# Kernel optimization log

Measured on AMD Instinct MI355X. Metric: run time of the kernel, lower is better.

The kernel has to match this reference:

```python
import jax, jax.numpy as jnp
import numpy as np

N = 100000   # nodes
E = 1600000  # edges
D = 128      # input feature dim
H = 128      # hidden dim
C = 40       # output classes


def _gcn_conv(x, W, b, src, dst, norm):
    # PyG GCNConv: h = x @ W; out_i = sum_j (d_i^-1/2 d_j^-1/2) h_j over in-edges,
    # including self-loops, then + bias. norm = deg^-1/2 with self-loop-augmented degree.
    h = x @ W                                    # [N, H]
    coef = norm[src] * norm[dst]                 # [E]
    agg = jax.ops.segment_sum(h[src] * coef[:, None], dst, num_segments=N)
    agg = agg + h * (norm * norm)[:, None]       # self-loop term
    return agg + b


def setup_inputs() -> dict:
    key = jax.random.key(0)
    ks = jax.random.split(key, 12)
    x = jax.random.normal(ks[0], (N, D), dtype=jnp.float32)
    edge_index = jax.random.randint(ks[1], (2, E), 0, N, dtype=jnp.int64)

    def lin(k, fan_in, fan_out):
        s = 1.0 / np.sqrt(fan_in)
        return jax.random.uniform(k, (fan_in, fan_out), jnp.float32, -s, s)

    return {
        "x": x,
        "edge_index": edge_index,
        "W1": lin(ks[2], D, H), "b1": jnp.zeros((H,), jnp.float32),
        "W2": lin(ks[3], H, H), "b2": jnp.zeros((H,), jnp.float32),
        "W3": lin(ks[4], H, H), "b3": jnp.zeros((H,), jnp.float32),
        "Wp1": lin(ks[5], H, H), "bp1": jnp.zeros((H,), jnp.float32),
        "Wp2": lin(ks[6], H, C), "bp2": jnp.zeros((C,), jnp.float32),
    }


def reference(x, edge_index, W1, b1, W2, b2, W3, b3, Wp1, bp1, Wp2, bp2):
    src, dst = edge_index[0], edge_index[1]
    # degree with self-loops (GCNConv adds self-loops by default)
    deg = jax.ops.segment_sum(jnp.ones((E,), jnp.float32), dst, num_segments=N) + 1.0
    norm = jax.lax.rsqrt(deg)                    # deg^-1/2

    h = x
    for W, b in ((W1, b1), (W2, b2), (W3, b3)):
        h = _gcn_conv(h, W, b, src, dst, norm)
        h = jax.nn.relu(h)
        # dropout is a no-op at inference / rate 0

    h = h @ Wp1 + bp1
    h = h @ Wp2 + bp2
    return jax.nn.log_softmax(h, axis=1)
```

## Files before the change

### kernel.cpp

```cpp
#include <hip/hip_runtime.h>
#include <hip/hip_bf16.h>
#include <math.h>


#define DH 128
#define NC 40
#define BN 128
#define MAXNB 1024
#define CAP 2560
#define CH 4096
#define SP 136

typedef __attribute__((ext_vector_type(8))) short bf16x8;
typedef __attribute__((ext_vector_type(4))) float f32x4;

__device__ __forceinline__ unsigned short f2bf(float f) {
    unsigned u = __float_as_uint(f);
    unsigned r = (u + 0x7fffu + ((u >> 16) & 1u)) >> 16;
    return (unsigned short)r;
}
__device__ __forceinline__ unsigned pack2(float lo, float hi) {
    return (unsigned)f2bf(lo) | ((unsigned)f2bf(hi) << 16);
}


__global__ __launch_bounds__(256) void init_bpos(unsigned* __restrict__ bpos, int NB) {
    int i = blockIdx.x * 256 + threadIdx.x;
    if (i < NB) bpos[i] = (unsigned)i * CAP;
}


__global__ __launch_bounds__(256) void bucket_scatter(const int* __restrict__ src,
                                                      const int* __restrict__ dst, int E,
                                                      unsigned* __restrict__ bpos,
                                                      unsigned* __restrict__ ebuf) {
    __shared__ unsigned hist[MAXNB];
    __shared__ unsigned gbase[MAXNB];
    __shared__ unsigned lim[MAXNB];
    __shared__ unsigned cur[MAXNB];
    int tid = threadIdx.x;
    int e0 = blockIdx.x * CH;
    int nE = min(CH, E - e0);
    int nE4 = nE & ~3;

    for (int i = tid; i < MAXNB; i += 256) { hist[i] = 0; cur[i] = 0; }
    __syncthreads();
    for (int i = tid * 4; i < nE4; i += 1024) {
        int4 dv = *(const int4*)(dst + e0 + i);
        atomicAdd(&hist[(unsigned)dv.x >> 7], 1u);
        atomicAdd(&hist[(unsigned)dv.y >> 7], 1u);
        atomicAdd(&hist[(unsigned)dv.z >> 7], 1u);
        atomicAdd(&hist[(unsigned)dv.w >> 7], 1u);
    }
    for (int i = nE4 + tid; i < nE; i += 256)
        atomicAdd(&hist[(unsigned)dst[e0 + i] >> 7], 1u);
    __syncthreads();
    for (int i = tid; i < MAXNB; i += 256) {
        unsigned h = hist[i];
        if (h) {
            unsigned o = atomicAdd(&bpos[i], h);
            gbase[i] = o;
            lim[i] = min(o + h, (unsigned)(i + 1) * CAP);
        }
    }
    __syncthreads();
    for (int i = tid * 4; i < nE4; i += 1024) {
        int4 sv = *(const int4*)(src + e0 + i);
        int4 dv = *(const int4*)(dst + e0 + i);
        {
            unsigned b = (unsigned)dv.x >> 7;
            unsigned p = gbase[b] + atomicAdd(&cur[b], 1u);
            if (p < lim[b]) ebuf[p] = ((unsigned)sv.x << 7) | ((unsigned)dv.x & 127u);
        }
        {
            unsigned b = (unsigned)dv.y >> 7;
            unsigned p = gbase[b] + atomicAdd(&cur[b], 1u);
            if (p < lim[b]) ebuf[p] = ((unsigned)sv.y << 7) | ((unsigned)dv.y & 127u);
        }
        {
            unsigned b = (unsigned)dv.z >> 7;
            unsigned p = gbase[b] + atomicAdd(&cur[b], 1u);
            if (p < lim[b]) ebuf[p] = ((unsigned)sv.z << 7) | ((unsigned)dv.z & 127u);
        }
        {
            unsigned b = (unsigned)dv.w >> 7;
            unsigned p = gbase[b] + atomicAdd(&cur[b], 1u);
            if (p < lim[b]) ebuf[p] = ((unsigned)sv.w << 7) | ((unsigned)dv.w & 127u);
        }
    }
    for (int i = nE4 + tid; i < nE; i += 256) {
        int s = src[e0 + i];
        int d = dst[e0 + i];
        unsigned b = (unsigned)d >> 7;
        unsigned p = gbase[b] + atomicAdd(&cur[b], 1u);
        if (p < lim[b]) ebuf[p] = ((unsigned)s << 7) | ((unsigned)d & 127u);
    }
}


__global__ __launch_bounds__(256) void bucket_degfill(const unsigned* __restrict__ ebuf,
                                                      const unsigned* __restrict__ bpos,
                                                      unsigned* __restrict__ cnt,
                                                      float* __restrict__ nrm,
                                                      unsigned* __restrict__ offN,
                                                      unsigned* __restrict__ dh,
                                                      int* __restrict__ csr, int N) {
    __shared__ unsigned h[BN], lb[BN], cur[BN];
    __shared__ int lcsr[CAP];
    __shared__ unsigned dhh[256];
    __shared__ unsigned tot;

    int b = blockIdx.x, tid = threadIdx.x;
    unsigned ebase = (unsigned)b * CAP;
    unsigned used = min(bpos[b] - ebase, (unsigned)CAP);
    unsigned used4 = used & ~3u;

    if (tid < BN) { h[tid] = 0; cur[tid] = 0; }
    dhh[tid] = 0;
    if (tid == 0) tot = 0;
    __syncthreads();

    for (unsigned i = tid * 4; i < used4; i += 1024) {
        uint4 v = *(const uint4*)(ebuf + ebase + i);
        atomicAdd(&h[v.x & 127u], 1u);
        atomicAdd(&h[v.y & 127u], 1u);
        atomicAdd(&h[v.z & 127u], 1u);
        atomicAdd(&h[v.w & 127u], 1u);
    }
    for (unsigned i = used4 + tid; i < used; i += 256)
        atomicAdd(&h[ebuf[ebase + i] & 127u], 1u);
    __syncthreads();

    if (tid < BN) {
        unsigned m = h[tid];
        lb[tid] = m ? atomicAdd(&tot, m) : 0u;
    }
    __syncthreads();

    for (unsigned i = tid * 4; i < used4; i += 1024) {
        uint4 v = *(const uint4*)(ebuf + ebase + i);
        {
            unsigned nl = v.x & 127u;
            unsigned r = atomicAdd(&cur[nl], 1u);
            lcsr[lb[nl] + r] = (int)(v.x >> 7);
        }
        {
            unsigned nl = v.y & 127u;
            unsigned r = atomicAdd(&cur[nl], 1u);
            lcsr[lb[nl] + r] = (int)(v.y >> 7);
        }
        {
            unsigned nl = v.z & 127u;
            unsigned r = atomicAdd(&cur[nl], 1u);
            lcsr[lb[nl] + r] = (int)(v.z >> 7);
        }
        {
            unsigned nl = v.w & 127u;
            unsigned r = atomicAdd(&cur[nl], 1u);
            lcsr[lb[nl] + r] = (int)(v.w >> 7);
        }
    }
    for (unsigned i = used4 + tid; i < used; i += 256) {
        unsigned v = ebuf[ebase + i];
        unsigned nl = v & 127u;
        unsigned r = atomicAdd(&cur[nl], 1u);
        lcsr[lb[nl] + r] = (int)(v >> 7);
    }

    if (tid < BN) {
        int node = b * BN + tid;
        if (node < N) {
            unsigned m = h[tid];
            cnt[node] = m;
            nrm[node] = rsqrtf((float)m + 1.0f);
            offN[node] = ebase + lb[tid];
            atomicAdd(&dhh[min(m, 255u)], 1u);
        }
    }
    __syncthreads();

    for (unsigned i = tid * 4; i < used4; i += 1024)
        *(int4*)(csr + ebase + i) = *(const int4*)&lcsr[i];
    for (unsigned i = used4 + tid; i < used; i += 256)
        csr[ebase + i] = lcsr[i];
    if (dhh[tid]) atomicAdd(&dh[tid], dhh[tid]);
}


__global__ __launch_bounds__(256) void deg_scatter(const unsigned* __restrict__ cnt, int N,
                                                   const unsigned* __restrict__ dh,
                                                   unsigned* __restrict__ binpos,
                                                   const unsigned* __restrict__ offN,
                                                   int* __restrict__ perm,
                                                   unsigned* __restrict__ pd2) {
    __shared__ unsigned hh[256], base[256], cur[256], sdh[256], sns[256];
    int t = threadIdx.x;
    hh[t] = 0; cur[t] = 0; sdh[t] = dh[t];
    __syncthreads();
    unsigned ns = 0;
    for (int d = t + 1; d < 256; ++d) ns += sdh[d];
    sns[t] = ns;
    int i = blockIdx.x * 256 + t;
    unsigned d = 0;
    if (i < N) { d = min(cnt[i], 255u); atomicAdd(&hh[d], 1u); }
    __syncthreads();
    if (hh[t]) base[t] = sns[t] + atomicAdd(&binpos[t], hh[t]);
    __syncthreads();
    if (i < N) {
        unsigned r = atomicAdd(&cur[d], 1u);
        unsigned idx = base[d] + r;
        perm[idx] = i;
        pd2[idx] = (offN[i] << 9) | min(cnt[i], 511u);
    }
}


__global__ __launch_bounds__(256) void prep_w(const float* __restrict__ W1,
                                              const float* __restrict__ W2,
                                              const float* __restrict__ W3,
                                              const float* __restrict__ Wp1,
                                              const float* __restrict__ bp1,
                                              const float* __restrict__ Wp2,
                                              const float* __restrict__ bp2,
                                              unsigned short* __restrict__ Wt,
                                              unsigned short* __restrict__ Wft,
                                              float* __restrict__ bfh) {
    int id = blockIdx.x * 256 + threadIdx.x;
    if (id < 3 * DH * DH) {
        int l = id >> 14, r = id & (DH * DH - 1);
        int k = r >> 7, n = r & 127;
        const float* W = (l == 0) ? W1 : (l == 1) ? W2 : W3;
        Wt[l * DH * DH + n * DH + k] = f2bf(W[k * DH + n]);
    } else if (id < 3 * DH * DH + 48 * DH) {
        int o = id - 3 * DH * DH;
        int c = o >> 7, k = o & 127;
        float acc = 0.f;
        if (c < NC)
            for (int j = 0; j < DH; ++j) acc += Wp1[k * DH + j] * Wp2[j * NC + c];
        Wft[c * DH + k] = f2bf(acc);
    } else if (id < 3 * DH * DH + 48 * DH + 48) {
        int c = id - 3 * DH * DH - 48 * DH;
        float acc = 0.f;
        if (c < NC) {
            acc = bp2[c];
            for (int j = 0; j < DH; ++j) acc += bp1[j] * Wp2[j * NC + c];
        }
        bfh[c] = acc;
    }
}


__global__ __launch_bounds__(256) void gemm_mfma_f32(const float* __restrict__ X,
                                                     const unsigned short* __restrict__ Wt,
                                                     const float* __restrict__ nrm,
                                                     unsigned short* __restrict__ outb,
                                                     int nrows) {
    const int tid = threadIdx.x;
    const int wave = tid >> 6;
    const int lane = tid & 63;
    const int m = lane & 15;
    const int quad = lane >> 4;
    const int rbase = blockIdx.x * 128 + wave * 32;

    union U8 { bf16x8 v; unsigned u[4]; };

    f32x4 acc[2][8];
#pragma unroll
    for (int rt = 0; rt < 2; ++rt)
#pragma unroll
        for (int ct = 0; ct < 8; ++ct) acc[rt][ct] = (f32x4){0.f, 0.f, 0.f, 0.f};

#pragma unroll
    for (int kt = 0; kt < 4; ++kt) {
        const int kof = kt * 32 + quad * 8;
        bf16x8 a[2], b[8];
#pragma unroll
        for (int rt = 0; rt < 2; ++rt) {
            int r = rbase + rt * 16 + m;
            r = (r < nrows) ? r : (nrows - 1);
            const float* p = X + (size_t)r * DH + kof;
            float4 u0 = *(const float4*)p;
            float4 u1 = *(const float4*)(p + 4);
            U8 t;
            t.u[0] = pack2(u0.x, u0.y);
            t.u[1] = pack2(u0.z, u0.w);
            t.u[2] = pack2(u1.x, u1.y);
            t.u[3] = pack2(u1.z, u1.w);
            a[rt] = t.v;
        }
#pragma unroll
        for (int ct = 0; ct < 8; ++ct)
            b[ct] = *(const bf16x8*)(Wt + (ct * 16 + m) * DH + kof);
#pragma unroll
        for (int rt = 0; rt < 2; ++rt)
#pragma unroll
            for (int ct = 0; ct < 8; ++ct)
                acc[rt][ct] = __builtin_amdgcn_mfma_f32_16x16x32_bf16(a[rt], b[ct], acc[rt][ct], 0, 0, 0);
    }

#pragma unroll
    for (int rt = 0; rt < 2; ++rt)
#pragma unroll
        for (int reg = 0; reg < 4; ++reg) {
            int r = rbase + rt * 16 + quad * 4 + reg;
            if (r < nrows) {
                float s = nrm[r];
#pragma unroll
                for (int ct = 0; ct < 8; ++ct)
                    outb[(size_t)r * DH + ct * 16 + m] = f2bf(acc[rt][ct][reg] * s);
            }
        }
}


__device__ __forceinline__ void bf8_add(float* acc, uint4 v) {
    acc[0] += __uint_as_float(v.x << 16);
    acc[1] += __uint_as_float(v.x & 0xffff0000u);
    acc[2] += __uint_as_float(v.y << 16);
    acc[3] += __uint_as_float(v.y & 0xffff0000u);
    acc[4] += __uint_as_float(v.z << 16);
    acc[5] += __uint_as_float(v.z & 0xffff0000u);
    acc[6] += __uint_as_float(v.w << 16);
    acc[7] += __uint_as_float(v.w & 0xffff0000u);
}

__device__ __forceinline__ void gather_phase(const uint4* __restrict__ Abf,
                                             const int* __restrict__ csr,
                                             const unsigned* __restrict__ pd2,
                                             const int* __restrict__ perm,
                                             const float* __restrict__ bias,
                                             unsigned short (*sA)[SP],
                                             int* snode, float* snrm, int N) {
    const int tid = threadIdx.x;
    const int g = tid >> 4;
    const int lane = tid & 15;
    const int idx = blockIdx.x * 16 + g;
    if (idx < N) {
        const unsigned pd = pd2[idx];
        const unsigned o = pd >> 9;
        const unsigned d = pd & 511u;
        const int node = perm[idx];

        int i0 = 0, i1 = 0, i2 = 0, i3 = 0;
        if ((unsigned)lane < d)      i0 = csr[o + lane];
        if ((unsigned)(16 + lane) < d) i1 = csr[o + 16 + lane];
        if ((unsigned)(32 + lane) < d) i2 = csr[o + 32 + lane];
        if ((unsigned)(48 + lane) < d) i3 = csr[o + 48 + lane];

        float acc[8];
        {
            uint4 v = Abf[(size_t)node * 16 + lane];
            acc[0] = __uint_as_float(v.x << 16);
            acc[1] = __uint_as_float(v.x & 0xffff0000u);
            acc[2] = __uint_as_float(v.y << 16);
            acc[3] = __uint_as_float(v.y & 0xffff0000u);
            acc[4] = __uint_as_float(v.z << 16);
            acc[5] = __uint_as_float(v.z & 0xffff0000u);
            acc[6] = __uint_as_float(v.w << 16);
            acc[7] = __uint_as_float(v.w & 0xffff0000u);
        }

        const unsigned dl = min(d, 64u);
        const int sb = g << 4;
        unsigned e = 0;
        for (; e + 4 <= dl; e += 4) {
            int rsel = (e < 16) ? i0 : (e < 32) ? i1 : (e < 48) ? i2 : i3;
            int bb = sb + (int)(e & 15u);
            int s0 = __shfl(rsel, bb + 0);
            int s1 = __shfl(rsel, bb + 1);
            int s2 = __shfl(rsel, bb + 2);
            int s3 = __shfl(rsel, bb + 3);
            uint4 v0 = Abf[(size_t)s0 * 16 + lane];
            uint4 v1 = Abf[(size_t)s1 * 16 + lane];
            uint4 v2 = Abf[(size_t)s2 * 16 + lane];
            uint4 v3 = Abf[(size_t)s3 * 16 + lane];
            bf8_add(acc, v0);
            bf8_add(acc, v1);
            bf8_add(acc, v2);
            bf8_add(acc, v3);
        }
        for (; e < dl; ++e) {
            int rsel = (e < 16) ? i0 : (e < 32) ? i1 : (e < 48) ? i2 : i3;
            int s = __shfl(rsel, sb + (int)(e & 15u));
            uint4 v = Abf[(size_t)s * 16 + lane];
            bf8_add(acc, v);
        }
        for (; e < d; ++e) {
            int s = csr[o + e];
            uint4 v = Abf[(size_t)s * 16 + lane];
            bf8_add(acc, v);
        }

        float nm = rsqrtf((float)d + 1.0f);
        if (lane == 0) { snode[g] = node; snrm[g] = nm; }
        float4 b0 = *(const float4*)(bias + lane * 8);
        float4 b1 = *(const float4*)(bias + lane * 8 + 4);
        uint4 ov;
        ov.x = pack2(fmaxf(acc[0] * nm + b0.x, 0.f), fmaxf(acc[1] * nm + b0.y, 0.f));
        ov.y = pack2(fmaxf(acc[2] * nm + b0.z, 0.f), fmaxf(acc[3] * nm + b0.w, 0.f));
        ov.z = pack2(fmaxf(acc[4] * nm + b1.x, 0.f), fmaxf(acc[5] * nm + b1.y, 0.f));
        ov.w = pack2(fmaxf(acc[6] * nm + b1.z, 0.f), fmaxf(acc[7] * nm + b1.w, 0.f));
        *(uint4*)&sA[g][lane * 8] = ov;
    }
    __syncthreads();
}


__global__ __launch_bounds__(256, 8) void agg_gemm(const uint4* __restrict__ Abf,
                                                   const int* __restrict__ csr,
                                                   const unsigned* __restrict__ pd2,
                                                   const int* __restrict__ perm,
                                                   const float* __restrict__ bias,
                                                   const unsigned short* __restrict__ Wt,
                                                   unsigned short* __restrict__ outb, int N) {
    __shared__ unsigned short sA[16][SP];
    __shared__ int snode[16];
    __shared__ float snrm[16];
    gather_phase(Abf, csr, pd2, perm, bias, sA, snode, snrm, N);

    const int tid = threadIdx.x;
    const int wave = tid >> 6;
    const int l64 = tid & 63;
    const int m = l64 & 15;
    const int quad = l64 >> 4;

    f32x4 acc[2];
    acc[0] = (f32x4){0.f, 0.f, 0.f, 0.f};
    acc[1] = (f32x4){0.f, 0.f, 0.f, 0.f};

#pragma unroll
    for (int kt = 0; kt < 4; ++kt) {
        const int kof = kt * 32 + quad * 8;
        bf16x8 a = *(const bf16x8*)&sA[m][kof];
#pragma unroll
        for (int c2 = 0; c2 < 2; ++c2) {
            const int ct = wave * 2 + c2;
            bf16x8 b = *(const bf16x8*)(Wt + (ct * 16 + m) * DH + kof);
            acc[c2] = __builtin_amdgcn_mfma_f32_16x16x32_bf16(a, b, acc[c2], 0, 0, 0);
        }
    }

#pragma unroll
    for (int reg = 0; reg < 4; ++reg) {
        int idx = blockIdx.x * 16 + quad * 4 + reg;
        if (idx < N) {
            int r = snode[quad * 4 + reg];
            float s = snrm[quad * 4 + reg];
#pragma unroll
            for (int c2 = 0; c2 < 2; ++c2)
                outb[(size_t)r * DH + (wave * 2 + c2) * 16 + m] = f2bf(acc[c2][reg] * s);
        }
    }
}


__global__ __launch_bounds__(256, 8) void agg_head(const uint4* __restrict__ Abf,
                                                   const int* __restrict__ csr,
                                                   const unsigned* __restrict__ pd2,
                                                   const int* __restrict__ perm,
                                                   const float* __restrict__ bias,
                                                   const unsigned short* __restrict__ Wft,
                                                   const float* __restrict__ bfh,
                                                   float* __restrict__ out, int N) {
    __shared__ unsigned short sA[16][SP];
    __shared__ int snode[16];
    __shared__ float snrm[16];
    gather_phase(Abf, csr, pd2, perm, bias, sA, snode, snrm, N);

    const int tid = threadIdx.x;
    if (tid >= 64) return;
    const int m = tid & 15;
    const int quad = tid >> 4;

    f32x4 acc[3];
#pragma unroll
    for (int ct = 0; ct < 3; ++ct) acc[ct] = (f32x4){0.f, 0.f, 0.f, 0.f};

#pragma unroll
    for (int kt = 0; kt < 4; ++kt) {
        const int kof = kt * 32 + quad * 8;
        bf16x8 a = *(const bf16x8*)&sA[m][kof];
#pragma unroll
        for (int ct = 0; ct < 3; ++ct) {
            bf16x8 b = *(const bf16x8*)(Wft + (ct * 16 + m) * DH + kof);
            acc[ct] = __builtin_amdgcn_mfma_f32_16x16x32_bf16(a, b, acc[ct], 0, 0, 0);
        }
    }

    float bias0 = bfh[m];
    float bias1 = bfh[16 + m];
    float bias2 = bfh[32 + m];

#pragma unroll
    for (int reg = 0; reg < 4; ++reg) {
        float v0 = acc[0][reg] + bias0;
        float v1 = acc[1][reg] + bias1;
        float v2 = (m < 8) ? (acc[2][reg] + bias2) : -1e30f;
        float mx = fmaxf(fmaxf(v0, v1), v2);
#pragma unroll
        for (int dlt = 1; dlt < 16; dlt <<= 1) mx = fmaxf(mx, __shfl_xor(mx, dlt));
        float s = __expf(v0 - mx) + __expf(v1 - mx) + ((m < 8) ? __expf(v2 - mx) : 0.f);
#pragma unroll
        for (int dlt = 1; dlt < 16; dlt <<= 1) s += __shfl_xor(s, dlt);
        float ls = mx + __logf(s);
        int idx = blockIdx.x * 16 + quad * 4 + reg;
        if (idx < N) {
            int r = snode[quad * 4 + reg];
            out[(size_t)r * NC + m] = v0 - ls;
            out[(size_t)r * NC + 16 + m] = v1 - ls;
            if (m < 8) out[(size_t)r * NC + 32 + m] = v2 - ls;
        }
    }
}


extern "C" void kernel_launch(void* const* d_in, const int* in_sizes, int n_in,
                              void* d_out, int out_size, void* d_ws, size_t ws_size,
                              hipStream_t stream) {
    const float* x   = (const float*)d_in[0];
    const int*   ei  = (const int*)d_in[1];
    const float* W1  = (const float*)d_in[2];
    const float* b1  = (const float*)d_in[3];
    const float* W2  = (const float*)d_in[4];
    const float* b2  = (const float*)d_in[5];
    const float* W3  = (const float*)d_in[6];
    const float* b3  = (const float*)d_in[7];
    const float* Wp1 = (const float*)d_in[8];
    const float* bp1 = (const float*)d_in[9];
    const float* Wp2 = (const float*)d_in[10];
    const float* bp2 = (const float*)d_in[11];
    float* out = (float*)d_out;

    const int N = in_sizes[0] / DH;
    const int E = in_sizes[1] / 2;
    const int* src = ei;
    const int* dst = ei + E;
    const int NB = (N + BN - 1) / BN;

    char* w = (char*)d_ws;
    unsigned short* Ab  = (unsigned short*)w; w += (size_t)N * DH * 2;
    unsigned short* Bb  = (unsigned short*)w; w += (size_t)N * DH * 2;
    int*      csr    = (int*)w;      w += (size_t)NB * CAP * 4;
    unsigned* ebuf   = (unsigned*)w; w += (size_t)NB * CAP * 4;
    unsigned* dh     = (unsigned*)w; w += 256 * 4;
    unsigned* binpos = (unsigned*)w; w += 256 * 4;
    unsigned* bpos   = (unsigned*)w; w += MAXNB * 4;
    unsigned* cnt    = (unsigned*)w; w += (size_t)N * 4;
    float*    nrm    = (float*)w;    w += (size_t)N * 4;
    unsigned* offN   = (unsigned*)w; w += (size_t)N * 4;
    unsigned* pd2    = (unsigned*)w; w += (size_t)((N + 31) & ~31) * 4;
    int*      perm   = (int*)w;      w += (size_t)((N + 31) & ~31) * 4;
    unsigned short* Wt  = (unsigned short*)w; w += 3 * DH * DH * 2;
    unsigned short* Wft = (unsigned short*)w; w += 48 * DH * 2;
    float*    bfh    = (float*)w;    w += 64 * 4;

    const int gC = (E + CH - 1) / CH;
    const int gN = (N + 255) / 256;

    hipMemsetAsync(dh, 0, 256 * 4 + 256 * 4, stream);
    init_bpos     <<<(NB + 255) / 256, 256, 0, stream>>>(bpos, NB);
    bucket_scatter<<<gC, 256, 0, stream>>>(src, dst, E, bpos, ebuf);
    bucket_degfill<<<NB, 256, 0, stream>>>(ebuf, bpos, cnt, nrm, offN, dh, csr, N);
    deg_scatter   <<<gN, 256, 0, stream>>>(cnt, N, dh, binpos, offN, perm, pd2);
    prep_w<<<(3 * DH * DH + 48 * DH + 48 + 255) / 256, 256, 0, stream>>>(
        W1, W2, W3, Wp1, bp1, Wp2, bp2, Wt, Wft, bfh);

    const int gG = (N + 127) / 128;
    const int gF = (N + 15) / 16;

    gemm_mfma_f32<<<gG, 256, 0, stream>>>(x, Wt, nrm, Ab, N);
    agg_gemm<<<gF, 256, 0, stream>>>((const uint4*)Ab, csr, pd2, perm, b1,
                                     Wt + DH * DH, Bb, N);
    agg_gemm<<<gF, 256, 0, stream>>>((const uint4*)Bb, csr, pd2, perm, b2,
                                     Wt + 2 * DH * DH, Ab, N);
    agg_head<<<gF, 256, 0, stream>>>((const uint4*)Ab, csr, pd2, perm, b3,
                                     Wft, bfh, out, N);
}
```

Before: 380.1 us.

## Merge weight prep into bucket scatter, drop init kernel, shrink GEMM tile

Folds the weight-prep kernel into the bucket scatter launch as extra blocks and replaces the bpos init kernel with a memset, so bucket offsets are now stored relative to each bucket's base. This removes two launches and their serialization gaps. The first-layer GEMM now gives each wave one 16-row tile instead of two, which doubles the grid and lowers register pressure. The explicit occupancy hint of 8 is also removed from the aggregation kernels, which may change their register allocation.

```diff
diff --git a/kernel.cpp b/kernel.cpp
--- a/kernel.cpp
+++ b/kernel.cpp
@@ -24,24 +24,49 @@
 }
 
 
-__global__ __launch_bounds__(256) void init_bpos(unsigned* __restrict__ bpos, int NB) {
-    int i = blockIdx.x * 256 + threadIdx.x;
-    if (i < NB) bpos[i] = (unsigned)i * CAP;
-}
-
-
-__global__ __launch_bounds__(256) void bucket_scatter(const int* __restrict__ src,
-                                                      const int* __restrict__ dst, int E,
-                                                      unsigned* __restrict__ bpos,
-                                                      unsigned* __restrict__ ebuf) {
+__global__ __launch_bounds__(256) void bucket_scatter_prep(
+        const int* __restrict__ src, const int* __restrict__ dst, int E,
+        unsigned* __restrict__ bpos, unsigned* __restrict__ ebuf,
+        const float* __restrict__ W1, const float* __restrict__ W2,
+        const float* __restrict__ W3, const float* __restrict__ Wp1,
+        const float* __restrict__ bp1, const float* __restrict__ Wp2,
+        const float* __restrict__ bp2, unsigned short* __restrict__ Wt,
+        unsigned short* __restrict__ Wft, float* __restrict__ bfh, int gC) {
     __shared__ unsigned hist[MAXNB];
     __shared__ unsigned gbase[MAXNB];
     __shared__ unsigned lim[MAXNB];
     __shared__ unsigned cur[MAXNB];
-    int tid = threadIdx.x;
-    int e0 = blockIdx.x * CH;
-    int nE = min(CH, E - e0);
-    int nE4 = nE & ~3;
+    const int tid = threadIdx.x;
+
+    if (blockIdx.x >= gC) {
+        int id = (blockIdx.x - gC) * 256 + tid;
+        if (id < 3 * DH * DH) {
+            int l = id >> 14, r = id & (DH * DH - 1);
+            int k = r >> 7, n = r & 127;
+            const float* W = (l == 0) ? W1 : (l == 1) ? W2 : W3;
+            Wt[l * DH * DH + n * DH + k] = f2bf(W[k * DH + n]);
+        } else if (id < 3 * DH * DH + 48 * DH) {
+            int o = id - 3 * DH * DH;
+            int c = o >> 7, k = o & 127;
+            float acc = 0.f;
+            if (c < NC)
+                for (int j = 0; j < DH; ++j) acc += Wp1[k * DH + j] * Wp2[j * NC + c];
+            Wft[c * DH + k] = f2bf(acc);
+        } else if (id < 3 * DH * DH + 48 * DH + 48) {
+            int c = id - 3 * DH * DH - 48 * DH;
+            float acc = 0.f;
+            if (c < NC) {
+                acc = bp2[c];
+                for (int j = 0; j < DH; ++j) acc += bp1[j] * Wp2[j * NC + c];
+            }
+            bfh[c] = acc;
+        }
+        return;
+    }
+
+    const int e0 = blockIdx.x * CH;
+    const int nE = min(CH, E - e0);
+    const int nE4 = nE & ~3;
 
     for (int i = tid; i < MAXNB; i += 256) { hist[i] = 0; cur[i] = 0; }
     __syncthreads();
@@ -58,7 +83,7 @@
     for (int i = tid; i < MAXNB; i += 256) {
         unsigned h = hist[i];
         if (h) {
-            unsigned o = atomicAdd(&bpos[i], h);
+            unsigned o = (unsigned)i * CAP + atomicAdd(&bpos[i], h);
             gbase[i] = o;
             lim[i] = min(o + h, (unsigned)(i + 1) * CAP);
         }
@@ -112,7 +137,7 @@
 
     int b = blockIdx.x, tid = threadIdx.x;
     unsigned ebase = (unsigned)b * CAP;
-    unsigned used = min(bpos[b] - ebase, (unsigned)CAP);
+    unsigned used = min(bpos[b], (unsigned)CAP);
     unsigned used4 = used & ~3u;
 
     if (tid < BN) { h[tid] = 0; cur[tid] = 0; }
@@ -211,41 +236,6 @@
         unsigned idx = base[d] + r;
         perm[idx] = i;
         pd2[idx] = (offN[i] << 9) | min(cnt[i], 511u);
-    }
-}
-
-
-__global__ __launch_bounds__(256) void prep_w(const float* __restrict__ W1,
-                                              const float* __restrict__ W2,
-                                              const float* __restrict__ W3,
-                                              const float* __restrict__ Wp1,
-                                              const float* __restrict__ bp1,
-                                              const float* __restrict__ Wp2,
-                                              const float* __restrict__ bp2,
-                                              unsigned short* __restrict__ Wt,
-                                              unsigned short* __restrict__ Wft,
-                                              float* __restrict__ bfh) {
-    int id = blockIdx.x * 256 + threadIdx.x;
-    if (id < 3 * DH * DH) {
-        int l = id >> 14, r = id & (DH * DH - 1);
-        int k = r >> 7, n = r & 127;
-        const float* W = (l == 0) ? W1 : (l == 1) ? W2 : W3;
-        Wt[l * DH * DH + n * DH + k] = f2bf(W[k * DH + n]);
-    } else if (id < 3 * DH * DH + 48 * DH) {
-        int o = id - 3 * DH * DH;
-        int c = o >> 7, k = o & 127;
-        float acc = 0.f;
-        if (c < NC)
-            for (int j = 0; j < DH; ++j) acc += Wp1[k * DH + j] * Wp2[j * NC + c];
-        Wft[c * DH + k] = f2bf(acc);
-    } else if (id < 3 * DH * DH + 48 * DH + 48) {
-        int c = id - 3 * DH * DH - 48 * DH;
-        float acc = 0.f;
-        if (c < NC) {
-            acc = bp2[c];
-            for (int j = 0; j < DH; ++j) acc += bp1[j] * Wp2[j * NC + c];
-        }
-        bfh[c] = acc;
     }
 }
 
@@ -260,56 +250,47 @@
     const int lane = tid & 63;
     const int m = lane & 15;
     const int quad = lane >> 4;
-    const int rbase = blockIdx.x * 128 + wave * 32;
+    const int rbase = blockIdx.x * 64 + wave * 16;
 
     union U8 { bf16x8 v; unsigned u[4]; };
 
-    f32x4 acc[2][8];
-#pragma unroll
-    for (int rt = 0; rt < 2; ++rt)
-#pragma unroll
-        for (int ct = 0; ct < 8; ++ct) acc[rt][ct] = (f32x4){0.f, 0.f, 0.f, 0.f};
+    f32x4 acc[8];
+#pragma unroll
+    for (int ct = 0; ct < 8; ++ct) acc[ct] = (f32x4){0.f, 0.f, 0.f, 0.f};
 
 #pragma unroll
     for (int kt = 0; kt < 4; ++kt) {
         const int kof = kt * 32 + quad * 8;
-        bf16x8 a[2], b[8];
-#pragma unroll
-        for (int rt = 0; rt < 2; ++rt) {
-            int r = rbase + rt * 16 + m;
-            r = (r < nrows) ? r : (nrows - 1);
-            const float* p = X + (size_t)r * DH + kof;
-            float4 u0 = *(const float4*)p;
-            float4 u1 = *(const float4*)(p + 4);
-            U8 t;
-            t.u[0] = pack2(u0.x, u0.y);
-            t.u[1] = pack2(u0.z, u0.w);
-            t.u[2] = pack2(u1.x, u1.y);
-            t.u[3] = pack2(u1.z, u1.w);
-            a[rt] = t.v;
-        }
+        int r = rbase + m;
+        r = (r < nrows) ? r : (nrows - 1);
+        const float* p = X + (size_t)r * DH + kof;
+        float4 u0 = *(const float4*)p;
+        float4 u1 = *(const float4*)(p + 4);
+        U8 t;
+        t.u[0] = pack2(u0.x, u0.y);
+        t.u[1] = pack2(u0.z, u0.w);
+        t.u[2] = pack2(u1.x, u1.y);
+        t.u[3] = pack2(u1.z, u1.w);
+        bf16x8 a = t.v;
+        bf16x8 b[8];
 #pragma unroll
         for (int ct = 0; ct < 8; ++ct)
             b[ct] = *(const bf16x8*)(Wt + (ct * 16 + m) * DH + kof);
 #pragma unroll
-        for (int rt = 0; rt < 2; ++rt)
+        for (int ct = 0; ct < 8; ++ct)
+            acc[ct] = __builtin_amdgcn_mfma_f32_16x16x32_bf16(a, b[ct], acc[ct], 0, 0, 0);
+    }
+
+#pragma unroll
+    for (int reg = 0; reg < 4; ++reg) {
+        int r = rbase + quad * 4 + reg;
+        if (r < nrows) {
+            float s = nrm[r];
 #pragma unroll
             for (int ct = 0; ct < 8; ++ct)
-                acc[rt][ct] = __builtin_amdgcn_mfma_f32_16x16x32_bf16(a[rt], b[ct], acc[rt][ct], 0, 0, 0);
-    }
-
-#pragma unroll
-    for (int rt = 0; rt < 2; ++rt)
-#pragma unroll
-        for (int reg = 0; reg < 4; ++reg) {
-            int r = rbase + rt * 16 + quad * 4 + reg;
-            if (r < nrows) {
-                float s = nrm[r];
-#pragma unroll
-                for (int ct = 0; ct < 8; ++ct)
-                    outb[(size_t)r * DH + ct * 16 + m] = f2bf(acc[rt][ct][reg] * s);
-            }
-        }
+                outb[(size_t)r * DH + ct * 16 + m] = f2bf(acc[ct][reg] * s);
+        }
+    }
 }
 
 
@@ -342,7 +323,7 @@
         const int node = perm[idx];
 
         int i0 = 0, i1 = 0, i2 = 0, i3 = 0;
-        if ((unsigned)lane < d)      i0 = csr[o + lane];
+        if ((unsigned)lane < d)        i0 = csr[o + lane];
         if ((unsigned)(16 + lane) < d) i1 = csr[o + 16 + lane];
         if ((unsigned)(32 + lane) < d) i2 = csr[o + 32 + lane];
         if ((unsigned)(48 + lane) < d) i3 = csr[o + 48 + lane];
@@ -406,13 +387,13 @@
 }
 
 
-__global__ __launch_bounds__(256, 8) void agg_gemm(const uint4* __restrict__ Abf,
-                                                   const int* __restrict__ csr,
-                                                   const unsigned* __restrict__ pd2,
-                                                   const int* __restrict__ perm,
-                                                   const float* __restrict__ bias,
-                                                   const unsigned short* __restrict__ Wt,
-                                                   unsigned short* __restrict__ outb, int N) {
+__global__ __launch_bounds__(256) void agg_gemm(const uint4* __restrict__ Abf,
+                                                const int* __restrict__ csr,
+                                                const unsigned* __restrict__ pd2,
+                                                const int* __restrict__ perm,
+                                                const float* __restrict__ bias,
+                                                const unsigned short* __restrict__ Wt,
+                                                unsigned short* __restrict__ outb, int N) {
     __shared__ unsigned short sA[16][SP];
     __shared__ int snode[16];
     __shared__ float snrm[16];
@@ -454,14 +435,14 @@
 }
 
 
-__global__ __launch_bounds__(256, 8) void agg_head(const uint4* __restrict__ Abf,
-                                                   const int* __restrict__ csr,
-                                                   const unsigned* __restrict__ pd2,
-                                                   const int* __restrict__ perm,
-                                                   const float* __restrict__ bias,
-                                                   const unsigned short* __restrict__ Wft,
-                                                   const float* __restrict__ bfh,
-                                                   float* __restrict__ out, int N) {
+__global__ __launch_bounds__(256) void agg_head(const uint4* __restrict__ Abf,
+                                                const int* __restrict__ csr,
+                                                const unsigned* __restrict__ pd2,
+                                                const int* __restrict__ perm,
+                                                const float* __restrict__ bias,
+                                                const unsigned short* __restrict__ Wft,
+                                                const float* __restrict__ bfh,
+                                                float* __restrict__ out, int N) {
     __shared__ unsigned short sA[16][SP];
     __shared__ int snode[16];
     __shared__ float snrm[16];
@@ -556,16 +537,16 @@
 
     const int gC = (E + CH - 1) / CH;
     const int gN = (N + 255) / 256;
-
-    hipMemsetAsync(dh, 0, 256 * 4 + 256 * 4, stream);
-    init_bpos     <<<(NB + 255) / 256, 256, 0, stream>>>(bpos, NB);
-    bucket_scatter<<<gC, 256, 0, stream>>>(src, dst, E, bpos, ebuf);
+    const int gP = (3 * DH * DH + 48 * DH + 48 + 255) / 256;
+
+    hipMemsetAsync(dh, 0, 256 * 4 + 256 * 4 + MAXNB * 4, stream);
+    bucket_scatter_prep<<<gC + gP, 256, 0, stream>>>(src, dst, E, bpos, ebuf,
+                                                     W1, W2, W3, Wp1, bp1, Wp2, bp2,
+                                                     Wt, Wft, bfh, gC);
     bucket_degfill<<<NB, 256, 0, stream>>>(ebuf, bpos, cnt, nrm, offN, dh, csr, N);
     deg_scatter   <<<gN, 256, 0, stream>>>(cnt, N, dh, binpos, offN, perm, pd2);
-    prep_w<<<(3 * DH * DH + 48 * DH + 48 + 255) / 256, 256, 0, stream>>>(
-        W1, W2, W3, Wp1, bp1, Wp2, bp2, Wt, Wft, bfh);
-
-    const int gG = (N + 127) / 128;
+
+    const int gG = (N + 63) / 64;
     const int gF = (N + 15) / 16;
 
     gemm_mfma_f32<<<gG, 256, 0, stream>>>(x, Wt, nrm, Ab, N);
```

Result: no change. 378.5 us (-0.4%).
